# Optimization experiments

Measured on AMD Instinct MI355X. Metric: run time of the kernel, lower is better.

Reference implementation:

```python
import jax, jax.numpy as jnp
import numpy as np

KH, KW, PAD, DIL, STRIDE = 3, 3, 1, 1, 1


def _conv2d(x, w):
    # plain dense conv, NCHW / OIHW, stride 1, pad 1
    return jax.lax.conv_general_dilated(
        x, w, window_strides=(STRIDE, STRIDE),
        padding=[(PAD, PAD), (PAD, PAD)],
        rhs_dilation=(DIL, DIL),
        dimension_numbers=('NCHW', 'OIHW', 'NCHW'))


def _deform_patches(x, offset):
    """Bilinear-sample deformable patches.
    x: [B,C,H,W], offset: [B,2K,Ho,Wo] with per-tap (dy,dx).
    Returns [B,C,K,Ho,Wo]."""
    B, C, H, W = x.shape
    Ho, Wo = offset.shape[2], offset.shape[3]
    K = KH * KW
    off = offset.reshape(B, K, 2, Ho, Wo)

    ky = jnp.repeat(jnp.arange(KH), KW)            # [K]
    kx = jnp.tile(jnp.arange(KW), KH)              # [K]
    base_y = (jnp.arange(Ho) * STRIDE - PAD)[None, :, None] + (DIL * ky)[:, None, None]  # [K,Ho,1]
    base_x = (jnp.arange(Wo) * STRIDE - PAD)[None, None, :] + (DIL * kx)[:, None, None]  # [K,1,Wo]

    sy = base_y[None].astype(x.dtype) + off[:, :, 0]   # [B,K,Ho,Wo]
    sx = base_x[None].astype(x.dtype) + off[:, :, 1]

    y0 = jnp.floor(sy); x0 = jnp.floor(sx)
    ly = sy - y0;       lx = sx - x0
    y0i = y0.astype(jnp.int32); x0i = x0.astype(jnp.int32)

    x_flat = x.reshape(B, C, H * W)

    def corner(yi, xi, wgt):
        valid = (yi >= 0) & (yi < H) & (xi >= 0) & (xi < W)   # zero padding outside
        idx = (jnp.clip(yi, 0, H - 1) * W + jnp.clip(xi, 0, W - 1))  # [B,K,Ho,Wo]
        gath = jax.vmap(lambda img, i: img[:, i.reshape(-1)])(x_flat, idx)  # [B,C,K*Ho*Wo]
        gath = gath.reshape(B, C, K, Ho, Wo)
        return gath * (wgt * valid.astype(x.dtype))[:, None]

    p = corner(y0i,     x0i,     (1 - ly) * (1 - lx))
    p = p + corner(y0i,     x0i + 1, (1 - ly) * lx)
    p = p + corner(y0i + 1, x0i,     ly * (1 - lx))
    p = p + corner(y0i + 1, x0i + 1, ly * lx)
    return p  # [B,C,K,Ho,Wo]


def setup_inputs() -> dict:
    key = jax.random.key(0)
    k1, k2, k3 = jax.random.split(key, 3)
    B, C, H, W = 8, 256, 64, 64
    Cout = 256
    x = jax.random.normal(k1, (B, C, H, W), dtype=jnp.float32)
    offset_w = jax.random.normal(k2, (2 * KH * KW, C, KH, KW), dtype=jnp.float32) * 0.02
    deform_w = jax.random.normal(k3, (Cout, C, KH, KW), dtype=jnp.float32) * 0.02
    return {"x": x, "offset_w": offset_w, "deform_w": deform_w}


def reference(x, offset_w, deform_w):
    # 1) offset-predicting conv
    offset = _conv2d(x, offset_w)                    # [B,2K,H,W]
    # 2) deformable conv = bilinear gather + contraction over (Cin, K)
    patches = _deform_patches(x, offset)             # [B,C,K,H,W]
    Cout = deform_w.shape[0]
    wk = deform_w.reshape(Cout, deform_w.shape[1], KH * KW)
    y = jnp.einsum('bckhw,ock->bohw', patches, wk)   # [B,Cout,H,W]
    # 3) avg + std channel attention (torch.std default: unbiased, ddof=1)
    avg = jnp.mean(y, axis=(2, 3), keepdims=True)
    std = jnp.std(y, axis=(2, 3), keepdims=True, ddof=1)
    attn = jax.nn.sigmoid(avg + std)
    return y * attn
```

## Files before the change

kernel.cpp:

```cpp
#include <hip/hip_runtime.h>
#include <hip/hip_bf16.h>
#include <math.h>

#define C_IN 256
#define H_   64
#define W_   64
#define B_   8
#define COUT 256
#define HW   (H_*W_)

typedef float f32x4 __attribute__((ext_vector_type(4)));
typedef float f32x2 __attribute__((ext_vector_type(2)));
typedef short short8 __attribute__((ext_vector_type(8)));

static __device__ __forceinline__ int pack_bf16x2(float a, float b) {
    __hip_bfloat162 h = __float22bfloat162_rn(make_float2(a, b));
    union { __hip_bfloat162 h; int i; } u; u.h = h;
    return u.i;
}

static __device__ __forceinline__ f32x2 up2(int v) {
    union { int i; float f; } a, b;
    a.i = v << 16;
    b.i = v & 0xffff0000;
    f32x2 r; r[0] = a.f; r[1] = b.f;
    return r;
}

__global__ __launch_bounds__(256) void prep_weights_kernel(
    const float* __restrict__ ow, const float* __restrict__ dw,
    short* __restrict__ wR, short* __restrict__ wO)
{
    int blk = blockIdx.x;
    int k   = blk / 288;
    int row = blk % 288;
    int c   = threadIdx.x;
    int cblk = c >> 6, ks = (c >> 5) & 1, q = (c >> 3) & 3, ce = c & 7;
    union { float f; unsigned u; } a;
    if (row < 256) {
        int o = row;
        a.f = dw[(size_t)o * 2304 + c * 9 + k];
        unsigned r = (a.u + 0x7fffu + ((a.u >> 16) & 1u)) >> 16;
        size_t idx = (size_t)(k * 8 + cblk * 2 + ks) * 8192
                   + (size_t)(o >> 4) * 512 + q * 128 + (o & 15) * 8 + ce;
        wR[idx] = (short)r;
    } else {
        int o = row - 256;
        a.f = (o < 18) ? ow[(size_t)o * 2304 + c * 9 + k] : 0.f;
        unsigned r = (a.u + 0x7fffu + ((a.u >> 16) & 1u)) >> 16;
        size_t idx = (size_t)(k * 8 + cblk * 2 + ks) * 1024
                   + (size_t)(o >> 4) * 512 + q * 128 + (o & 15) * 8 + ce;
        wO[idx] = (short)r;
    }
}

__global__ __launch_bounds__(256) void transpose_x_kernel(
    const float* __restrict__ x, unsigned short* __restrict__ xT)
{
    __shared__ float tile[64][257];
    const int tid = threadIdx.x;
    const int b = blockIdx.x >> 6, h = blockIdx.x & 63;
    const float* xb = x + ((size_t)b << 20) + h * 64;

#pragma unroll
    for (int pass = 0; pass < 16; ++pass) {
        int c  = pass * 16 + (tid >> 4);
        int w0 = (tid & 15) * 4;
        float4 v = *(const float4*)(xb + (size_t)c * 4096 + w0);
        tile[w0][c] = v.x; tile[w0 + 1][c] = v.y;
        tile[w0 + 2][c] = v.z; tile[w0 + 3][c] = v.w;
    }
    __syncthreads();

    int4* ob = (int4*)(xT + ((size_t)blockIdx.x << 14));
#pragma unroll
    for (int pass = 0; pass < 8; ++pass) {
        int idx = pass * 256 + tid;
        int w = idx >> 5, ch8 = idx & 31;
        const float* tr = &tile[w][ch8 * 8];
        int4 pk;
        pk.x = pack_bf16x2(tr[0], tr[1]);
        pk.y = pack_bf16x2(tr[2], tr[3]);
        pk.z = pack_bf16x2(tr[4], tr[5]);
        pk.w = pack_bf16x2(tr[6], tr[7]);
        ob[idx] = pk;
    }
}

__global__ __launch_bounds__(256, 2) void offset_mfma_kernel(
    const unsigned short* __restrict__ xT, const short* __restrict__ wO,
    float* __restrict__ offs)
{
    __shared__ int4 bT[2][64 * 8];

    const int tid = threadIdx.x;
    const int b   = blockIdx.x & 7;
    const int ho  = blockIdx.x >> 3;

    const int px = tid >> 2;
    const int cg = tid & 3;
    const int wv = tid >> 6;
    const int ln = tid & 63;
    const int lo = ln & 15;
    const int quad = ln >> 4;
    const int pxl = wv * 16 + lo;

    f32x4 acc[2];
    acc[0] = (f32x4){0.f, 0.f, 0.f, 0.f};
    acc[1] = (f32x4){0.f, 0.f, 0.f, 0.f};

    const unsigned short* xbb = xT + ((size_t)b << 20);
    const int4 zero4 = {0, 0, 0, 0};

    auto stageB = [&](int s, int buf) {
        int k = s >> 2, c0 = (s & 3) << 6;
        int yy = ho + k / 3 - 1;
        int xx = px + k % 3 - 1;
        bool valid = (yy >= 0) & (yy < 64) & (xx >= 0) & (xx < 64);
        int yc = min(max(yy, 0), 63), xc = min(max(xx, 0), 63);
        const int4* src = (const int4*)(xbb + (((size_t)yc * 64 + xc) << 8) + c0 + cg * 16);
        int4 p0 = valid ? src[0] : zero4;
        int4 p1 = valid ? src[1] : zero4;
        bT[buf][px * 8 + ((2 * cg)     ^ (px & 7))] = p0;
        bT[buf][px * 8 + ((2 * cg + 1) ^ (px & 7))] = p1;
    };

    stageB(0, 0);
    __syncthreads();

    for (int s = 0; s < 36; ++s) {
        const int cur = s & 1;
        if (s < 35) stageB(s + 1, cur ^ 1);

        const int k = s >> 2;
        const short* wkb = wO + (size_t)(k * 8 + (s & 3) * 2) * 1024 + ln * 8;
#pragma unroll
        for (int ks = 0; ks < 2; ++ks) {
            int ch = ks * 4 + quad;
            short8 bfr = *(const short8*)&bT[cur][pxl * 8 + (ch ^ (pxl & 7))];
#pragma unroll
            for (int t = 0; t < 2; ++t) {
                short8 afr = *(const short8*)(wkb + ks * 1024 + t * 512);
                acc[t] = __builtin_amdgcn_mfma_f32_16x16x32_bf16(afr, bfr, acc[t], 0, 0, 0);
            }
        }
        __syncthreads();
    }

#pragma unroll
    for (int t = 0; t < 2; ++t) {
#pragma unroll
        for (int r = 0; r < 4; ++r) {
            int o = t * 16 + quad * 4 + r;
            if (o < 18)
                offs[((size_t)b * 18 + o) * HW + ho * 64 + wv * 16 + lo] = acc[t][r];
        }
    }
}

__global__ __launch_bounds__(256, 2) void deform_mfma_kernel(
    const unsigned short* __restrict__ xT, const float* __restrict__ offs,
    const short* __restrict__ wR, float* __restrict__ y,
    float* __restrict__ sum_, float* __restrict__ sumsq_)
{
    __shared__ int4   meta_i[576];
    __shared__ float4 meta_w[576];
    __shared__ int4   bT[2][64 * 8];

    const int tid = threadIdx.x;
    const int b   = blockIdx.x & 7;
    const int ho  = blockIdx.x >> 3;

    for (int e = tid; e < 576; e += 256) {
        int kk  = e >> 6;
        int pxe = e & 63;
        float dy = offs[((size_t)b * 18 + 2 * kk)     * HW + ho * W_ + pxe];
        float dx = offs[((size_t)b * 18 + 2 * kk + 1) * HW + ho * W_ + pxe];
        float sy = (float)(ho - 1 + kk / 3) + dy;
        float sx = (float)(pxe - 1 + kk % 3) + dx;
        float y0f = floorf(sy), x0f = floorf(sx);
        float ly = sy - y0f, lx = sx - x0f;
        int y0 = (int)y0f, x0 = (int)x0f;
        int y1 = y0 + 1, x1 = x0 + 1;
        float wy0 = 1.f - ly, wx0 = 1.f - lx;
        bool vy0 = (y0 >= 0) & (y0 < H_), vy1 = (y1 >= 0) & (y1 < H_);
        bool vx0 = (x0 >= 0) & (x0 < W_), vx1 = (x1 >= 0) & (x1 < W_);
        int cy0 = min(max(y0, 0), H_ - 1), cy1 = min(max(y1, 0), H_ - 1);
        int cx0 = min(max(x0, 0), W_ - 1), cx1 = min(max(x1, 0), W_ - 1);
        int4 ii; float4 ww;
        ii.x = cy0 * W_ + cx0;  ww.x = wy0 * wx0 * ((vy0 & vx0) ? 1.f : 0.f);
        ii.y = cy0 * W_ + cx1;  ww.y = wy0 * lx  * ((vy0 & vx1) ? 1.f : 0.f);
        ii.z = cy1 * W_ + cx0;  ww.z = ly  * wx0 * ((vy1 & vx0) ? 1.f : 0.f);
        ii.w = cy1 * W_ + cx1;  ww.w = ly  * lx  * ((vy1 & vx1) ? 1.f : 0.f);
        meta_i[e] = ii;
        meta_w[e] = ww;
    }

    const int px = tid >> 2;
    const int cg = tid & 3;
    const int wv = tid >> 6;
    const int ln = tid & 63;
    const int lo = ln & 15;
    const int quad = ln >> 4;

    f32x4 acc[4][4];
#pragma unroll
    for (int t = 0; t < 4; ++t)
#pragma unroll
        for (int p = 0; p < 4; ++p)
            acc[t][p] = (f32x4){0.f, 0.f, 0.f, 0.f};

    const unsigned short* xbb = xT + ((size_t)b << 20) + cg * 16;

#define ISSUE_G(S, G0,G1,G2,G3,G4,G5,G6,G7)                                   \
    {                                                                         \
        int kn_ = (S) >> 2, cn_ = ((S) & 3) << 6;                             \
        int4 ii_ = meta_i[kn_ * 64 + px];                                     \
        const unsigned short* xc_ = xbb + cn_;                                \
        const int4* pA_ = (const int4*)(xc_ + ((size_t)ii_.x << 8));          \
        const int4* pB_ = (const int4*)(xc_ + ((size_t)ii_.y << 8));          \
        const int4* pC_ = (const int4*)(xc_ + ((size_t)ii_.z << 8));          \
        const int4* pD_ = (const int4*)(xc_ + ((size_t)ii_.w << 8));          \
        G0 = pA_[0]; G1 = pA_[1];                                             \
        G2 = pB_[0]; G3 = pB_[1];                                             \
        G4 = pC_[0]; G5 = pC_[1];                                             \
        G6 = pD_[0]; G7 = pD_[1];                                             \
    }

#define BLEND_W(S, BUF, G0,G1,G2,G3,G4,G5,G6,G7)                              \
    {                                                                         \
        int kn_ = (S) >> 2;                                                   \
        float4 w4_ = meta_w[kn_ * 64 + px];                                   \
        auto bl_ = [&](int av, int bv, int cv, int dv) -> int {               \
            f32x2 r_ = up2(av) * w4_.x + up2(bv) * w4_.y                      \
                     + up2(cv) * w4_.z + up2(dv) * w4_.w;                     \
            return pack_bf16x2(r_[0], r_[1]);                                 \
        };                                                                    \
        int4 o0_, o1_;                                                        \
        o0_.x = bl_(G0.x, G2.x, G4.x, G6.x);                                  \
        o0_.y = bl_(G0.y, G2.y, G4.y, G6.y);                                  \
        o0_.z = bl_(G0.z, G2.z, G4.z, G6.z);                                  \
        o0_.w = bl_(G0.w, G2.w, G4.w, G6.w);                                  \
        o1_.x = bl_(G1.x, G3.x, G5.x, G7.x);                                  \
        o1_.y = bl_(G1.y, G3.y, G5.y, G7.y);                                  \
        o1_.z = bl_(G1.z, G3.z, G5.z, G7.z);                                  \
        o1_.w = bl_(G1.w, G3.w, G5.w, G7.w);                                  \
        bT[BUF][px * 8 + ((2 * cg)     ^ (px & 7))] = o0_;                    \
        bT[BUF][px * 8 + ((2 * cg + 1) ^ (px & 7))] = o1_;                    \
    }

    auto mfmaStage = [&](int s, int buf) {
        const int k = s >> 2;
        const short* wkb = wR + (size_t)(k * 8 + (s & 3) * 2) * 8192
                         + wv * 2048 + ln * 8;
        short8 afr[2][4];
#pragma unroll
        for (int ks = 0; ks < 2; ++ks)
#pragma unroll
            for (int t = 0; t < 4; ++t)
                afr[ks][t] = *(const short8*)(wkb + ks * 8192 + t * 512);
        __builtin_amdgcn_s_setprio(1);
#pragma unroll
        for (int ks = 0; ks < 2; ++ks) {
            int ch = ks * 4 + quad;
            short8 bfr[4];
#pragma unroll
            for (int p = 0; p < 4; ++p) {
                int pp = p * 16 + lo;
                bfr[p] = *(const short8*)&bT[buf][pp * 8 + (ch ^ (pp & 7))];
            }
#pragma unroll
            for (int t = 0; t < 4; ++t)
#pragma unroll
                for (int p = 0; p < 4; ++p)
                    acc[t][p] = __builtin_amdgcn_mfma_f32_16x16x32_bf16(
                        afr[ks][t], bfr[p], acc[t][p], 0, 0, 0);
        }
        __builtin_amdgcn_s_setprio(0);
    };

    int4 a0, a1, a2, a3, a4, a5, a6, a7;
    int4 b0, b1, b2, b3, b4, b5, b6, b7;

    __syncthreads();

    ISSUE_G(0, a0,a1,a2,a3,a4,a5,a6,a7);
    ISSUE_G(1, b0,b1,b2,b3,b4,b5,b6,b7);
    BLEND_W(0, 0, a0,a1,a2,a3,a4,a5,a6,a7);
    __syncthreads();

#pragma unroll 1
    for (int t = 0; t < 17; ++t) {
        int s = 2 * t;
        ISSUE_G(s + 2, a0,a1,a2,a3,a4,a5,a6,a7);
        __builtin_amdgcn_sched_barrier(0);
        mfmaStage(s, 0);
        BLEND_W(s + 1, 1, b0,b1,b2,b3,b4,b5,b6,b7);
        __syncthreads();
        ISSUE_G(s + 3, b0,b1,b2,b3,b4,b5,b6,b7);
        __builtin_amdgcn_sched_barrier(0);
        mfmaStage(s + 1, 1);
        BLEND_W(s + 2, 0, a0,a1,a2,a3,a4,a5,a6,a7);
        __syncthreads();
    }
    mfmaStage(34, 0);
    BLEND_W(35, 1, b0,b1,b2,b3,b4,b5,b6,b7);
    __syncthreads();
    mfmaStage(35, 1);

#undef ISSUE_G
#undef BLEND_W

    float* yb = y + ((size_t)b << 20) + ho * 64;
#pragma unroll
    for (int t = 0; t < 4; ++t) {
#pragma unroll
        for (int r = 0; r < 4; ++r) {
            int o = wv * 64 + t * 16 + quad * 4 + r;
            float sv = 0.f, qv = 0.f;
#pragma unroll
            for (int p = 0; p < 4; ++p) {
                float val = acc[t][p][r];
                yb[(size_t)o * HW + p * 16 + lo] = val;
                sv += val;
                qv += val * val;
            }
#pragma unroll
            for (int m = 1; m <= 8; m <<= 1) {
                sv += __shfl_xor(sv, m, 16);
                qv += __shfl_xor(qv, m, 16);
            }
            if (lo == 0) {
                atomicAdd(&sum_[b * COUT + o], sv);
                atomicAdd(&sumsq_[b * COUT + o], qv);
            }
        }
    }
}

__global__ __launch_bounds__(256) void attn_scale_kernel(
    const float* __restrict__ sum_, const float* __restrict__ sumsq_,
    float* __restrict__ y)
{
    int bo = blockIdx.x;
    float s = sum_[bo], q = sumsq_[bo];
    float mean = s * (1.f / 4096.f);
    float var  = (q - s * s * (1.f / 4096.f)) * (1.f / 4095.f);
    float sd   = sqrtf(fmaxf(var, 0.f));
    float attn = 1.f / (1.f + expf(-(mean + sd)));
    float4* yp = (float4*)(y + (size_t)bo * HW);
#pragma unroll
    for (int i = 0; i < 4; ++i) {
        float4 v = yp[threadIdx.x + i * 256];
        v.x *= attn; v.y *= attn; v.z *= attn; v.w *= attn;
        yp[threadIdx.x + i * 256] = v;
    }
}

extern "C" void kernel_launch(void* const* d_in, const int* in_sizes, int n_in,
                              void* d_out, int out_size, void* d_ws, size_t ws_size,
                              hipStream_t stream)
{
    const float* x  = (const float*)d_in[0];
    const float* ow = (const float*)d_in[1];
    const float* dw = (const float*)d_in[2];
    float* out = (float*)d_out;
    float* ws  = (float*)d_ws;

    float*          offs = ws;
    unsigned short* xT   = (unsigned short*)(ws + 589824);
    short*          wR   = (short*)(xT + 8388608);
    short*          wO   = wR + 589824;
    float*          sum_ = (float*)(wO + 73728);
    float*          sumsq_ = sum_ + 2048;

    hipMemsetAsync(sum_, 0, 2 * 2048 * sizeof(float), stream);

    prep_weights_kernel<<<9 * 288, 256, 0, stream>>>(ow, dw, wR, wO);
    transpose_x_kernel<<<512, 256, 0, stream>>>(x, xT);
    offset_mfma_kernel<<<512, 256, 0, stream>>>(xT, wO, offs);
    deform_mfma_kernel<<<512, 256, 0, stream>>>(xT, offs, wR, out, sum_, sumsq_);
    attn_scale_kernel<<<2048, 256, 0, stream>>>(sum_, sumsq_, out);
}
```

Before: 188.0 us.

## Software-pipeline weight fragment loads and offset-conv gathers one stage ahead

The offset conv kernel is restructured into a register-prefetch pipeline: global loads of the next stage's input and weight fragments are issued before the current MFMA stage, and results are committed to LDS afterward. The deform kernel likewise prefetches weight fragments one stage ahead in registers instead of loading them right before the MFMAs. It also precomputes byte offsets (index<<9) in the metadata so fewer address shifts are needed per gather. This hides global load latency behind MFMA work at the cost of more live registers, which could cause spills or lower occupancy.

```diff
diff --git a/kernel.cpp b/kernel.cpp
--- a/kernel.cpp
+++ b/kernel.cpp
@@ -87,6 +87,8 @@
     }
 }
 
+struct ofrag { short8 v[2][2]; };
+
 __global__ __launch_bounds__(256, 2) void offset_mfma_kernel(
     const unsigned short* __restrict__ xT, const short* __restrict__ wO,
     float* __restrict__ offs)
@@ -112,40 +114,84 @@
     const unsigned short* xbb = xT + ((size_t)b << 20);
     const int4 zero4 = {0, 0, 0, 0};
 
-    auto stageB = [&](int s, int buf) {
-        int k = s >> 2, c0 = (s & 3) << 6;
-        int yy = ho + k / 3 - 1;
-        int xx = px + k % 3 - 1;
-        bool valid = (yy >= 0) & (yy < 64) & (xx >= 0) & (xx < 64);
-        int yc = min(max(yy, 0), 63), xc = min(max(xx, 0), 63);
-        const int4* src = (const int4*)(xbb + (((size_t)yc * 64 + xc) << 8) + c0 + cg * 16);
-        int4 p0 = valid ? src[0] : zero4;
-        int4 p1 = valid ? src[1] : zero4;
-        bT[buf][px * 8 + ((2 * cg)     ^ (px & 7))] = p0;
-        bT[buf][px * 8 + ((2 * cg + 1) ^ (px & 7))] = p1;
-    };
-
-    stageB(0, 0);
-    __syncthreads();
-
-    for (int s = 0; s < 36; ++s) {
-        const int cur = s & 1;
-        if (s < 35) stageB(s + 1, cur ^ 1);
-
-        const int k = s >> 2;
-        const short* wkb = wO + (size_t)(k * 8 + (s & 3) * 2) * 1024 + ln * 8;
+#define WO_ISSUE(S, WF)                                                       \
+    {                                                                         \
+        const short* wkb_ = wO + (size_t)((((S) >> 2) * 8 + ((S) & 3) * 2))   \
+                          * 1024 + ln * 8;                                    \
+        _Pragma("unroll")                                                     \
+        for (int ks_ = 0; ks_ < 2; ++ks_)                                     \
+            _Pragma("unroll")                                                 \
+            for (int t_ = 0; t_ < 2; ++t_)                                    \
+                WF.v[ks_][t_] = *(const short8*)(wkb_ + ks_ * 1024 + t_ * 512);\
+    }
+
+#define O_ISSUE(S, P0, P1)                                                    \
+    {                                                                         \
+        int k_ = (S) >> 2, c0_ = ((S) & 3) << 6;                              \
+        int yy_ = ho + k_ / 3 - 1;                                            \
+        int xx_ = px + k_ % 3 - 1;                                            \
+        int yc_ = min(max(yy_, 0), 63), xc_ = min(max(xx_, 0), 63);           \
+        const int4* src_ = (const int4*)(xbb + (((size_t)yc_ * 64 + xc_) << 8)\
+                                         + c0_ + cg * 16);                    \
+        P0 = src_[0]; P1 = src_[1];                                           \
+    }
+#define O_COMMIT(S, BUF, P0, P1)                                              \
+    {                                                                         \
+        int k_ = (S) >> 2;                                                    \
+        int yy_ = ho + k_ / 3 - 1;                                            \
+        int xx_ = px + k_ % 3 - 1;                                            \
+        bool v_ = (yy_ >= 0) & (yy_ < 64) & (xx_ >= 0) & (xx_ < 64);          \
+        bT[BUF][px * 8 + ((2 * cg)     ^ (px & 7))] = v_ ? P0 : zero4;        \
+        bT[BUF][px * 8 + ((2 * cg + 1) ^ (px & 7))] = v_ ? P1 : zero4;        \
+    }
+
+    auto mfmaO = [&](int buf, const ofrag& WF) {
+        __builtin_amdgcn_s_setprio(1);
 #pragma unroll
         for (int ks = 0; ks < 2; ++ks) {
             int ch = ks * 4 + quad;
-            short8 bfr = *(const short8*)&bT[cur][pxl * 8 + (ch ^ (pxl & 7))];
-#pragma unroll
-            for (int t = 0; t < 2; ++t) {
-                short8 afr = *(const short8*)(wkb + ks * 1024 + t * 512);
-                acc[t] = __builtin_amdgcn_mfma_f32_16x16x32_bf16(afr, bfr, acc[t], 0, 0, 0);
-            }
+            short8 bfr = *(const short8*)&bT[buf][pxl * 8 + (ch ^ (pxl & 7))];
+#pragma unroll
+            for (int t = 0; t < 2; ++t)
+                acc[t] = __builtin_amdgcn_mfma_f32_16x16x32_bf16(
+                    WF.v[ks][t], bfr, acc[t], 0, 0, 0);
         }
+        __builtin_amdgcn_s_setprio(0);
+    };
+
+    int4 pa0, pa1, pb0, pb1;
+    ofrag wfA, wfB;
+    WO_ISSUE(0, wfA);
+    O_ISSUE(0, pa0, pa1);
+    O_ISSUE(1, pb0, pb1);
+    O_COMMIT(0, 0, pa0, pa1);
+    __syncthreads();
+
+#pragma unroll 1
+    for (int t = 0; t < 17; ++t) {
+        int s = 2 * t;
+        WO_ISSUE(s + 1, wfB);
+        O_ISSUE(s + 2, pa0, pa1);
+        __builtin_amdgcn_sched_barrier(0);
+        mfmaO(0, wfA);
+        O_COMMIT(s + 1, 1, pb0, pb1);
         __syncthreads();
-    }
+        WO_ISSUE(s + 2, wfA);
+        O_ISSUE(s + 3, pb0, pb1);
+        __builtin_amdgcn_sched_barrier(0);
+        mfmaO(1, wfB);
+        O_COMMIT(s + 2, 0, pa0, pa1);
+        __syncthreads();
+    }
+    WO_ISSUE(35, wfB);
+    __builtin_amdgcn_sched_barrier(0);
+    mfmaO(0, wfA);
+    O_COMMIT(35, 1, pb0, pb1);
+    __syncthreads();
+    mfmaO(1, wfB);
+#undef WO_ISSUE
+#undef O_ISSUE
+#undef O_COMMIT
 
 #pragma unroll
     for (int t = 0; t < 2; ++t) {
@@ -157,6 +203,8 @@
         }
     }
 }
+
+struct afrag { short8 v[2][4]; };
 
 __global__ __launch_bounds__(256, 2) void deform_mfma_kernel(
     const unsigned short* __restrict__ xT, const float* __restrict__ offs,
@@ -188,10 +236,10 @@
         int cy0 = min(max(y0, 0), H_ - 1), cy1 = min(max(y1, 0), H_ - 1);
         int cx0 = min(max(x0, 0), W_ - 1), cx1 = min(max(x1, 0), W_ - 1);
         int4 ii; float4 ww;
-        ii.x = cy0 * W_ + cx0;  ww.x = wy0 * wx0 * ((vy0 & vx0) ? 1.f : 0.f);
-        ii.y = cy0 * W_ + cx1;  ww.y = wy0 * lx  * ((vy0 & vx1) ? 1.f : 0.f);
-        ii.z = cy1 * W_ + cx0;  ww.z = ly  * wx0 * ((vy1 & vx0) ? 1.f : 0.f);
-        ii.w = cy1 * W_ + cx1;  ww.w = ly  * lx  * ((vy1 & vx1) ? 1.f : 0.f);
+        ii.x = (cy0 * W_ + cx0) << 9;  ww.x = wy0 * wx0 * ((vy0 & vx0) ? 1.f : 0.f);
+        ii.y = (cy0 * W_ + cx1) << 9;  ww.y = wy0 * lx  * ((vy0 & vx1) ? 1.f : 0.f);
+        ii.z = (cy1 * W_ + cx0) << 9;  ww.z = ly  * wx0 * ((vy1 & vx0) ? 1.f : 0.f);
+        ii.w = (cy1 * W_ + cx1) << 9;  ww.w = ly  * lx  * ((vy1 & vx1) ? 1.f : 0.f);
         meta_i[e] = ii;
         meta_w[e] = ww;
     }
@@ -210,21 +258,32 @@
         for (int p = 0; p < 4; ++p)
             acc[t][p] = (f32x4){0.f, 0.f, 0.f, 0.f};
 
-    const unsigned short* xbb = xT + ((size_t)b << 20) + cg * 16;
+    const char* xbb = (const char*)(xT + ((size_t)b << 20) + cg * 16);
 
 #define ISSUE_G(S, G0,G1,G2,G3,G4,G5,G6,G7)                                   \
     {                                                                         \
-        int kn_ = (S) >> 2, cn_ = ((S) & 3) << 6;                             \
+        int kn_ = (S) >> 2, cn_ = ((S) & 3) << 7;                             \
         int4 ii_ = meta_i[kn_ * 64 + px];                                     \
-        const unsigned short* xc_ = xbb + cn_;                                \
-        const int4* pA_ = (const int4*)(xc_ + ((size_t)ii_.x << 8));          \
-        const int4* pB_ = (const int4*)(xc_ + ((size_t)ii_.y << 8));          \
-        const int4* pC_ = (const int4*)(xc_ + ((size_t)ii_.z << 8));          \
-        const int4* pD_ = (const int4*)(xc_ + ((size_t)ii_.w << 8));          \
+        const char* xc_ = xbb + cn_;                                          \
+        const int4* pA_ = (const int4*)(xc_ + ii_.x);                         \
+        const int4* pB_ = (const int4*)(xc_ + ii_.y);                         \
+        const int4* pC_ = (const int4*)(xc_ + ii_.z);                         \
+        const int4* pD_ = (const int4*)(xc_ + ii_.w);                         \
         G0 = pA_[0]; G1 = pA_[1];                                             \
         G2 = pB_[0]; G3 = pB_[1];                                             \
         G4 = pC_[0]; G5 = pC_[1];                                             \
         G6 = pD_[0]; G7 = pD_[1];                                             \
+    }
+
+#define ISSUE_A(S, AF)                                                        \
+    {                                                                         \
+        const short* wkb_ = wR + (size_t)((((S) >> 2) * 8 + ((S) & 3) * 2))   \
+                          * 8192 + wv * 2048 + ln * 8;                        \
+        _Pragma("unroll")                                                     \
+        for (int ks_ = 0; ks_ < 2; ++ks_)                                     \
+            _Pragma("unroll")                                                 \
+            for (int t_ = 0; t_ < 4; ++t_)                                    \
+                AF.v[ks_][t_] = *(const short8*)(wkb_ + ks_ * 8192 + t_ * 512);\
     }
 
 #define BLEND_W(S, BUF, G0,G1,G2,G3,G4,G5,G6,G7)                              \
@@ -249,16 +308,7 @@
         bT[BUF][px * 8 + ((2 * cg + 1) ^ (px & 7))] = o1_;                    \
     }
 
-    auto mfmaStage = [&](int s, int buf) {
-        const int k = s >> 2;
-        const short* wkb = wR + (size_t)(k * 8 + (s & 3) * 2) * 8192
-                         + wv * 2048 + ln * 8;
-        short8 afr[2][4];
-#pragma unroll
-        for (int ks = 0; ks < 2; ++ks)
-#pragma unroll
-            for (int t = 0; t < 4; ++t)
-                afr[ks][t] = *(const short8*)(wkb + ks * 8192 + t * 512);
+    auto mfmaStage = [&](int buf, const afrag& AF) {
         __builtin_amdgcn_s_setprio(1);
 #pragma unroll
         for (int ks = 0; ks < 2; ++ks) {
@@ -274,16 +324,18 @@
 #pragma unroll
                 for (int p = 0; p < 4; ++p)
                     acc[t][p] = __builtin_amdgcn_mfma_f32_16x16x32_bf16(
-                        afr[ks][t], bfr[p], acc[t][p], 0, 0, 0);
+                        AF.v[ks][t], bfr[p], acc[t][p], 0, 0, 0);
         }
         __builtin_amdgcn_s_setprio(0);
     };
 
     int4 a0, a1, a2, a3, a4, a5, a6, a7;
     int4 b0, b1, b2, b3, b4, b5, b6, b7;
-
-    __syncthreads();
-
+    afrag afrA, afrB;
+
+    __syncthreads();
+
+    ISSUE_A(0, afrA);
     ISSUE_G(0, a0,a1,a2,a3,a4,a5,a6,a7);
     ISSUE_G(1, b0,b1,b2,b3,b4,b5,b6,b7);
     BLEND_W(0, 0, a0,a1,a2,a3,a4,a5,a6,a7);
@@ -292,23 +344,28 @@
 #pragma unroll 1
     for (int t = 0; t < 17; ++t) {
         int s = 2 * t;
+        ISSUE_A(s + 1, afrB);
         ISSUE_G(s + 2, a0,a1,a2,a3,a4,a5,a6,a7);
         __builtin_amdgcn_sched_barrier(0);
-        mfmaStage(s, 0);
+        mfmaStage(0, afrA);
         BLEND_W(s + 1, 1, b0,b1,b2,b3,b4,b5,b6,b7);
         __syncthreads();
+        ISSUE_A(s + 2, afrA);
         ISSUE_G(s + 3, b0,b1,b2,b3,b4,b5,b6,b7);
         __builtin_amdgcn_sched_barrier(0);
-        mfmaStage(s + 1, 1);
+        mfmaStage(1, afrB);
         BLEND_W(s + 2, 0, a0,a1,a2,a3,a4,a5,a6,a7);
         __syncthreads();
     }
-    mfmaStage(34, 0);
+    ISSUE_A(35, afrB);
+    __builtin_amdgcn_sched_barrier(0);
+    mfmaStage(0, afrA);
     BLEND_W(35, 1, b0,b1,b2,b3,b4,b5,b6,b7);
     __syncthreads();
-    mfmaStage(35, 1);
+    mfmaStage(1, afrB);
 
 #undef ISSUE_G
+#undef ISSUE_A
 #undef BLEND_W
 
     float* yb = y + ((size_t)b << 20) + ho * 64;
```

Measured after the change: 214.1 us. +13.9%, slower.

## Prefetch weight fragments one stage ahead and use LDS-only barriers

Applied to the files above, without the earlier changes.

Weight A-fragment loads from global memory are moved out of the MFMA stage and issued one stage early into double-buffered register structs, so their latency overlaps the previous stage's MFMAs. Gather offsets are precomputed as byte offsets in the metadata, which removes per-load shifts. __syncthreads is replaced by a barrier that waits only on lgkmcnt (LDS), so in-flight global gathers are not drained at each barrier. This raises register pressure under launch bounds of 2 blocks per SIMD, and correctness depends on the global loads being waited on before use.

```diff
diff --git a/kernel.cpp b/kernel.cpp
--- a/kernel.cpp
+++ b/kernel.cpp
@@ -25,6 +25,12 @@
     b.i = v & 0xffff0000;
     f32x2 r; r[0] = a.f; r[1] = b.f;
     return r;
+}
+
+static __device__ __forceinline__ void wg_barrier_lds() {
+    asm volatile("s_waitcnt lgkmcnt(0)" ::: "memory");
+    __builtin_amdgcn_s_barrier();
+    __builtin_amdgcn_sched_barrier(0);
 }
 
 __global__ __launch_bounds__(256) void prep_weights_kernel(
@@ -158,6 +164,8 @@
     }
 }
 
+struct afrag { short8 v[2][4]; };
+
 __global__ __launch_bounds__(256, 2) void deform_mfma_kernel(
     const unsigned short* __restrict__ xT, const float* __restrict__ offs,
     const short* __restrict__ wR, float* __restrict__ y,
@@ -188,10 +196,10 @@
         int cy0 = min(max(y0, 0), H_ - 1), cy1 = min(max(y1, 0), H_ - 1);
         int cx0 = min(max(x0, 0), W_ - 1), cx1 = min(max(x1, 0), W_ - 1);
         int4 ii; float4 ww;
-        ii.x = cy0 * W_ + cx0;  ww.x = wy0 * wx0 * ((vy0 & vx0) ? 1.f : 0.f);
-        ii.y = cy0 * W_ + cx1;  ww.y = wy0 * lx  * ((vy0 & vx1) ? 1.f : 0.f);
-        ii.z = cy1 * W_ + cx0;  ww.z = ly  * wx0 * ((vy1 & vx0) ? 1.f : 0.f);
-        ii.w = cy1 * W_ + cx1;  ww.w = ly  * lx  * ((vy1 & vx1) ? 1.f : 0.f);
+        ii.x = (cy0 * W_ + cx0) << 9;  ww.x = wy0 * wx0 * ((vy0 & vx0) ? 1.f : 0.f);
+        ii.y = (cy0 * W_ + cx1) << 9;  ww.y = wy0 * lx  * ((vy0 & vx1) ? 1.f : 0.f);
+        ii.z = (cy1 * W_ + cx0) << 9;  ww.z = ly  * wx0 * ((vy1 & vx0) ? 1.f : 0.f);
+        ii.w = (cy1 * W_ + cx1) << 9;  ww.w = ly  * lx  * ((vy1 & vx1) ? 1.f : 0.f);
         meta_i[e] = ii;
         meta_w[e] = ww;
     }
@@ -210,21 +218,32 @@
         for (int p = 0; p < 4; ++p)
             acc[t][p] = (f32x4){0.f, 0.f, 0.f, 0.f};
 
-    const unsigned short* xbb = xT + ((size_t)b << 20) + cg * 16;
+    const char* xbb = (const char*)(xT + ((size_t)b << 20) + cg * 16);
 
 #define ISSUE_G(S, G0,G1,G2,G3,G4,G5,G6,G7)                                   \
     {                                                                         \
-        int kn_ = (S) >> 2, cn_ = ((S) & 3) << 6;                             \
+        int kn_ = (S) >> 2, cn_ = ((S) & 3) << 7;                             \
         int4 ii_ = meta_i[kn_ * 64 + px];                                     \
-        const unsigned short* xc_ = xbb + cn_;                                \
-        const int4* pA_ = (const int4*)(xc_ + ((size_t)ii_.x << 8));          \
-        const int4* pB_ = (const int4*)(xc_ + ((size_t)ii_.y << 8));          \
-        const int4* pC_ = (const int4*)(xc_ + ((size_t)ii_.z << 8));          \
-        const int4* pD_ = (const int4*)(xc_ + ((size_t)ii_.w << 8));          \
+        const char* xc_ = xbb + cn_;                                          \
+        const int4* pA_ = (const int4*)(xc_ + ii_.x);                         \
+        const int4* pB_ = (const int4*)(xc_ + ii_.y);                         \
+        const int4* pC_ = (const int4*)(xc_ + ii_.z);                         \
+        const int4* pD_ = (const int4*)(xc_ + ii_.w);                         \
         G0 = pA_[0]; G1 = pA_[1];                                             \
         G2 = pB_[0]; G3 = pB_[1];                                             \
         G4 = pC_[0]; G5 = pC_[1];                                             \
         G6 = pD_[0]; G7 = pD_[1];                                             \
+    }
+
+#define ISSUE_A(S, AF)                                                        \
+    {                                                                         \
+        const short* wkb_ = wR + (size_t)((((S) >> 2) * 8 + ((S) & 3) * 2))   \
+                          * 8192 + wv * 2048 + ln * 8;                        \
+        _Pragma("unroll")                                                     \
+        for (int ks_ = 0; ks_ < 2; ++ks_)                                     \
+            _Pragma("unroll")                                                 \
+            for (int t_ = 0; t_ < 4; ++t_)                                    \
+                AF.v[ks_][t_] = *(const short8*)(wkb_ + ks_ * 8192 + t_ * 512);\
     }
 
 #define BLEND_W(S, BUF, G0,G1,G2,G3,G4,G5,G6,G7)                              \
@@ -249,16 +268,7 @@
         bT[BUF][px * 8 + ((2 * cg + 1) ^ (px & 7))] = o1_;                    \
     }
 
-    auto mfmaStage = [&](int s, int buf) {
-        const int k = s >> 2;
-        const short* wkb = wR + (size_t)(k * 8 + (s & 3) * 2) * 8192
-                         + wv * 2048 + ln * 8;
-        short8 afr[2][4];
-#pragma unroll
-        for (int ks = 0; ks < 2; ++ks)
-#pragma unroll
-            for (int t = 0; t < 4; ++t)
-                afr[ks][t] = *(const short8*)(wkb + ks * 8192 + t * 512);
+    auto mfmaStage = [&](int buf, const afrag& AF) {
         __builtin_amdgcn_s_setprio(1);
 #pragma unroll
         for (int ks = 0; ks < 2; ++ks) {
@@ -274,41 +284,48 @@
 #pragma unroll
                 for (int p = 0; p < 4; ++p)
                     acc[t][p] = __builtin_amdgcn_mfma_f32_16x16x32_bf16(
-                        afr[ks][t], bfr[p], acc[t][p], 0, 0, 0);
+                        AF.v[ks][t], bfr[p], acc[t][p], 0, 0, 0);
         }
         __builtin_amdgcn_s_setprio(0);
     };
 
     int4 a0, a1, a2, a3, a4, a5, a6, a7;
     int4 b0, b1, b2, b3, b4, b5, b6, b7;
-
-    __syncthreads();
-
+    afrag afrA, afrB;
+
+    wg_barrier_lds();
+
+    ISSUE_A(0, afrA);
     ISSUE_G(0, a0,a1,a2,a3,a4,a5,a6,a7);
     ISSUE_G(1, b0,b1,b2,b3,b4,b5,b6,b7);
     BLEND_W(0, 0, a0,a1,a2,a3,a4,a5,a6,a7);
-    __syncthreads();
+    wg_barrier_lds();
 
 #pragma unroll 1
     for (int t = 0; t < 17; ++t) {
         int s = 2 * t;
+        ISSUE_A(s + 1, afrB);
         ISSUE_G(s + 2, a0,a1,a2,a3,a4,a5,a6,a7);
         __builtin_amdgcn_sched_barrier(0);
-        mfmaStage(s, 0);
+        mfmaStage(0, afrA);
         BLEND_W(s + 1, 1, b0,b1,b2,b3,b4,b5,b6,b7);
-        __syncthreads();
+        wg_barrier_lds();
+        ISSUE_A(s + 2, afrA);
         ISSUE_G(s + 3, b0,b1,b2,b3,b4,b5,b6,b7);
         __builtin_amdgcn_sched_barrier(0);
-        mfmaStage(s + 1, 1);
+        mfmaStage(1, afrB);
         BLEND_W(s + 2, 0, a0,a1,a2,a3,a4,a5,a6,a7);
-        __syncthreads();
-    }
-    mfmaStage(34, 0);
+        wg_barrier_lds();
+    }
+    ISSUE_A(35, afrB);
+    __builtin_amdgcn_sched_barrier(0);
+    mfmaStage(0, afrA);
     BLEND_W(35, 1, b0,b1,b2,b3,b4,b5,b6,b7);
-    __syncthreads();
-    mfmaStage(35, 1);
+    wg_barrier_lds();
+    mfmaStage(1, afrB);
 
 #undef ISSUE_G
+#undef ISSUE_A
 #undef BLEND_W
 
     float* yb = y + ((size_t)b << 20) + ho * 64;
```

Result: no change. 187.2 us (-0.4%).
